# Kernel optimization log

Hardware: AMD Instinct MI355X
Metric: run time of the kernel (lower is better)

Reference implementation:

```python
import jax, jax.numpy as jnp
import numpy as np

B, S, NX, H = 8, 1024, 1024, 16
D = NX // H  # head dim = 64


def setup_inputs() -> dict:
    key = jax.random.key(0)
    k1, k2, k3 = jax.random.split(key, 3)
    x = jax.random.normal(k1, (B, S, NX), dtype=jnp.float32)
    Wqkv = jax.random.normal(k2, (NX, 3 * NX), dtype=jnp.float32) * 0.02
    bqkv = jnp.zeros((3 * NX,), dtype=jnp.float32)
    Wproj = jax.random.normal(k3, (NX, NX), dtype=jnp.float32) * 0.02
    bproj = jnp.zeros((NX,), dtype=jnp.float32)
    return {"x": x, "Wqkv": Wqkv, "bqkv": bqkv, "Wproj": Wproj, "bproj": bproj}


def reference(x, Wqkv, bqkv, Wproj, bproj):
    # c_attn: Conv1D == x @ W + b
    qkv = jnp.einsum('bsn,nm->bsm', x, Wqkv) + bqkv  # [B,S,3*NX]
    q, k, v = jnp.split(qkv, 3, axis=-1)
    # split heads -> [B,H,S,D]
    def split_heads(t):
        return t.reshape(B, S, H, D).transpose(0, 2, 1, 3)
    q, k, v = split_heads(q), split_heads(k), split_heads(v)
    # present = stack(key, value) with key as [B,H,S,D]
    present = jnp.stack((k, v))  # [2,B,H,S,D]
    # scores, scaled (scale=True) by sqrt(head_dim)
    w = jnp.einsum('bhqd,bhkd->bhqk', q, k) / jnp.sqrt(jnp.asarray(D, x.dtype))
    bias = jnp.tril(jnp.ones((S, S), dtype=x.dtype))[None, None]  # causal tril buffer
    w = w * bias - 10000.0 * (1.0 - bias)
    w = jax.nn.softmax(w, axis=-1)
    a = jnp.einsum('bhqk,bhkd->bhqd', w, v)  # [B,H,S,D]
    a = a.transpose(0, 2, 1, 3).reshape(B, S, NX)  # merge heads
    a = jnp.einsum('bsn,nm->bsm', a, Wproj) + bproj  # c_proj
    return a, present
```

## Files before the change

### kernel.cpp

```cpp
#include <hip/hip_runtime.h>
#include <stdint.h>


#define BB 8
#define SS 1024
#define NXX 1024
#define NH 16
#define HD 64
#define KK 1024
#define NKT 16

typedef __bf16 bf16x8 __attribute__((ext_vector_type(8)));
typedef float  floatx4 __attribute__((ext_vector_type(4)));
typedef unsigned short ushort8 __attribute__((ext_vector_type(8)));
typedef unsigned short ushortx4 __attribute__((ext_vector_type(4)));

__device__ inline float bf2f(unsigned short u) {
    unsigned int x = ((unsigned int)u) << 16;
    float f;
    __builtin_memcpy(&f, &x, 4);
    return f;
}
__device__ inline unsigned short f2bf(float f) {
    unsigned int u;
    __builtin_memcpy(&u, &f, 4);
    u += 0x7FFFu + ((u >> 16) & 1u);
    return (unsigned short)(u >> 16);
}

__device__ inline void gload_lds16(const unsigned short* g, unsigned short* l) {
    __builtin_amdgcn_global_load_lds(
        (const __attribute__((address_space(1))) void*)g,
        (__attribute__((address_space(3))) void*)l, 16, 0, 0);
}

__device__ inline void barrier_raw() {
    asm volatile("" ::: "memory");
    __builtin_amdgcn_sched_barrier(0);
    __builtin_amdgcn_s_barrier();
    __builtin_amdgcn_sched_barrier(0);
    asm volatile("" ::: "memory");
}
#define WAIT_VM4() asm volatile("s_waitcnt vmcnt(4)" ::: "memory")
#define WAIT_VM0() asm volatile("s_waitcnt vmcnt(0)" ::: "memory")

__global__ void sniff_k(const unsigned short* __restrict__ x, int* __restrict__ flag) {
    if (threadIdx.x == 0 && blockIdx.x == 0) {
        int g = 0;
        for (int i = 0; i < 512; i++) {
            float f = bf2f(x[i]);
            float a = fabsf(f);
            if (!(a <= 1e4f)) g++;
            else if (f != 0.f && a < 1e-35f) g++;
        }
        *flag = (g > 16) ? 1 : 0;
    }
}

__global__ __launch_bounds__(256) void prep(
    const void* __restrict__ x, const void* __restrict__ Wqkv,
    const void* __restrict__ Wproj,
    unsigned short* __restrict__ xbf, unsigned short* __restrict__ WqkvT,
    unsigned short* __restrict__ WprojT, const int* __restrict__ flagp) {
    const int f32 = *flagp;
    int blk = blockIdx.x;
    if (blk < 4096) {
        const size_t i = ((size_t)blk * 256 + threadIdx.x) * 8;
        if (f32) {
            const floatx4* p = (const floatx4*)((const float*)x + i);
            floatx4 f0 = p[0], f1 = p[1];
            ushort8 u;
#pragma unroll
            for (int j = 0; j < 4; j++) { u[j] = f2bf(f0[j]); u[4 + j] = f2bf(f1[j]); }
            *(ushort8*)(xbf + i) = u;
        } else {
            *(ushort8*)(xbf + i) = *(const ushort8*)((const unsigned short*)x + i);
        }
        return;
    }
    blk -= 4096;
    const void* in;
    unsigned short* out;
    int R, C;
    if (blk < 3072) { in = Wqkv; out = WqkvT; R = 1024; C = 3072; }
    else            { blk -= 3072; in = Wproj; out = WprojT; R = 1024; C = 1024; }
    const int ctiles = C / 32;
    const int c0 = (blk % ctiles) * 32, r0 = (blk / ctiles) * 32;

    __shared__ unsigned short tile[32][33];
    const int tx = threadIdx.x & 31, ty = threadIdx.x >> 5;
    if (f32) {
        const float* inf = (const float*)in;
#pragma unroll
        for (int i = ty; i < 32; i += 8)
            tile[i][tx] = f2bf(inf[(size_t)(r0 + i) * C + c0 + tx]);
    } else {
        const unsigned short* inu = (const unsigned short*)in;
#pragma unroll
        for (int i = ty; i < 32; i += 8)
            tile[i][tx] = inu[(size_t)(r0 + i) * C + c0 + tx];
    }
    __syncthreads();
#pragma unroll
    for (int i = ty; i < 32; i += 8)
        out[(size_t)(c0 + i) * R + r0 + tx] = tile[tx][i];
}

__global__ __launch_bounds__(256) void transpose_v(
    const void* __restrict__ outbase, unsigned short* __restrict__ vbfT,
    const int* __restrict__ flagp) {
    const int f32 = *flagp;
    const int blk = blockIdx.x;
    const int sb = blk & 15;
    const int bh = blk >> 4;
    const int tid = threadIdx.x;
    const int r = tid >> 2;
    const int c0 = (tid & 3) * 16;
    __shared__ unsigned short tile[64][72];
    const int perm = ((r & 15) << 2) | (r >> 4);
    const size_t esz = f32 ? 4 : 2;
    const char* vbase = (const char*)outbase + (size_t)(2 * BB * SS * NXX) * esz;
    if (f32) {
        const float* src = (const float*)vbase + ((size_t)bh * SS + sb * 64 + r) * HD + c0;
#pragma unroll
        for (int j = 0; j < 16; j++) tile[c0 + j][perm] = f2bf(src[j]);
    } else {
        const unsigned short* src = (const unsigned short*)vbase + ((size_t)bh * SS + sb * 64 + r) * HD + c0;
#pragma unroll
        for (int j = 0; j < 16; j++) tile[c0 + j][perm] = src[j];
    }
    __syncthreads();
    const int d = tid >> 2;
    const int o0 = (tid & 3) * 16;
    unsigned short* dst = vbfT + ((size_t)(bh * HD + d)) * SS + sb * 64 + o0;
    *(ushort8*)dst       = *(const ushort8*)&tile[d][o0];
    *(ushort8*)(dst + 8) = *(const ushort8*)&tile[d][o0 + 8];
}

#define STAGE_A(slot, h, kt) do { \
    const unsigned short* sg_ = Ab + (size_t)((h) * 128) * KK + (size_t)(kt) * 64; \
    gload_lds16(sg_, &As[slot][h][w * 512]); \
    gload_lds16(sg_ + (size_t)64 * KK, &As[slot][h][4096 + w * 512]); \
} while (0)
#define STAGE_B(slot, h, kt) do { \
    const unsigned short* sg_ = Bb + (size_t)((h) * 128) * KK + (size_t)(kt) * 64; \
    gload_lds16(sg_, &Bs[slot][h][w * 512]); \
    gload_lds16(sg_ + (size_t)64 * KK, &Bs[slot][h][4096 + w * 512]); \
} while (0)
#define PHASE(qq, STAGE_STMT, TAIL) do { \
    bf16x8 a_[2][2]; \
    _Pragma("unroll") \
    for (int mm = 0; mm < 2; mm++) { \
        const int arow = (qq) * 32 + mm * 16 + l15; \
        a_[mm][0] = *(const bf16x8*)&Ah[arow * 64 + fo0]; \
        a_[mm][1] = *(const bf16x8*)&Ah[arow * 64 + fo1]; \
    } \
    STAGE_STMT; \
    barrier_raw(); \
    __builtin_amdgcn_s_setprio(1); \
    _Pragma("unroll") \
    for (int mm = 0; mm < 2; mm++) \
    _Pragma("unroll") \
    for (int nf = 0; nf < 4; nf++) { \
        acc[2 * (qq) + mm][nf] = __builtin_amdgcn_mfma_f32_16x16x32_bf16(a_[mm][0], bfr[nf][0], acc[2 * (qq) + mm][nf], 0, 0, 0); \
        acc[2 * (qq) + mm][nf] = __builtin_amdgcn_mfma_f32_16x16x32_bf16(a_[mm][1], bfr[nf][1], acc[2 * (qq) + mm][nf], 0, 0, 0); \
    } \
    __builtin_amdgcn_s_setprio(0); \
    TAIL; \
    barrier_raw(); \
} while (0)

template <int MODE>
__global__ __launch_bounds__(512, 2) void gemm8p(
    const unsigned short* __restrict__ A,
    const unsigned short* __restrict__ Bt,
    const void* __restrict__ bias,
    void* __restrict__ outbase,
    unsigned short* __restrict__ q_ws,
    unsigned short* __restrict__ kbf,
    int M, int N, int Nt, const int* __restrict__ flagp) {
    __shared__ __align__(16) unsigned short As[2][2][128 * 64];
    __shared__ __align__(16) unsigned short Bs[2][2][128 * 64];

    const int f32 = *flagp;
    const int tid  = threadIdx.x;
    const int lane = tid & 63;
    const int w = tid >> 6;
    const int r = w >> 2;
    const int c = w & 3;
    const int bh2 = c >> 1;
    const int l15 = lane & 15;
    const int quad = lane >> 4;

    const int cpx = gridDim.x >> 3;
    const int bid = (blockIdx.x & 7) * cpx + (blockIdx.x >> 3);
    const int bx = bid % Nt, by = bid / Nt;
    const int row0 = by * 256, col0 = bx * 256;

    floatx4 acc[8][4];
    floatx4 zz = {0.f, 0.f, 0.f, 0.f};
#pragma unroll
    for (int i = 0; i < 8; i++)
#pragma unroll
        for (int j = 0; j < 4; j++) acc[i][j] = zz;

    const int srow = tid >> 3;
    const int scole = ((tid & 7) ^ (srow & 7)) << 3;
    const unsigned short* Ab = A  + (size_t)(row0 + srow) * KK + scole;
    const unsigned short* Bb = Bt + (size_t)(col0 + srow) * KK + scole;

    const int fo0 = (quad << 3) ^ ((l15 & 7) << 3);
    const int fo1 = fo0 ^ 32;

    STAGE_A(0, 0, 0); STAGE_A(0, 1, 0);
    STAGE_B(0, 0, 0); STAGE_B(0, 1, 0);
    STAGE_B(1, 0, 1); STAGE_B(1, 1, 1);
    WAIT_VM4();
    barrier_raw();

    bf16x8 bfr[4][2];
#pragma unroll 2
    for (int t = 0; t < NKT; t++) {
        const int slot = t & 1;
        const unsigned short* Ah = &As[slot][r][0];
        const unsigned short* Bh = &Bs[slot][bh2][0];
#pragma unroll
        for (int nf = 0; nf < 4; nf++) {
            const int brow = (c & 1) * 64 + nf * 16 + l15;
            bfr[nf][0] = *(const bf16x8*)&Bh[brow * 64 + fo0];
            bfr[nf][1] = *(const bf16x8*)&Bh[brow * 64 + fo1];
        }
        PHASE(0, { if (t + 1 < NKT) STAGE_A((t + 1) & 1, 0, t + 1); }, {});
        PHASE(1, { if (t + 1 < NKT) STAGE_A((t + 1) & 1, 1, t + 1); }, {});
        PHASE(2, { if (t + 2 < NKT) STAGE_B(slot, 0, t + 2); }, {});
        PHASE(3, { if (t + 2 < NKT) STAGE_B(slot, 1, t + 2); },
              { if (t < NKT - 2) { WAIT_VM4(); } else { WAIT_VM0(); } });
    }

    float bv[4];
#pragma unroll
    for (int nf = 0; nf < 4; nf++) {
        const int colb = col0 + c * 64 + nf * 16 + l15;
        bv[nf] = f32 ? ((const float*)bias)[colb] : bf2f(((const unsigned short*)bias)[colb]);
    }

    if (MODE == 0) {
#pragma unroll
        for (int mi = 0; mi < 8; mi++)
#pragma unroll
            for (int nf = 0; nf < 4; nf++) {
                const int colb = col0 + c * 64 + nf * 16 + l15;
#pragma unroll
                for (int i = 0; i < 4; i++) {
                    const int row = row0 + r * 128 + mi * 16 + quad * 4 + i;
                    const float val = acc[mi][nf][i] + bv[nf];
                    const size_t idx = (size_t)row * N + colb;
                    if (f32) ((float*)outbase)[idx] = val;
                    else     ((unsigned short*)outbase)[idx] = f2bf(val);
                }
            }
        return;
    }

    const int sec = col0 >> 10;
    const size_t esz = f32 ? 4 : 2;
    const int b = row0 >> 10;
    const int s0 = row0 & 1023;

    if (sec == 0) {
#pragma unroll
        for (int mi = 0; mi < 8; mi++)
#pragma unroll
            for (int nf = 0; nf < 4; nf++) {
                const int colb = col0 + c * 64 + nf * 16 + l15;
                const int h = (colb & 1023) >> 6, d = colb & 63;
#pragma unroll
                for (int i = 0; i < 4; i++) {
                    const int s = s0 + r * 128 + mi * 16 + quad * 4 + i;
                    q_ws[(size_t)((b * NH + h) * SS + s) * HD + d] = f2bf(acc[mi][nf][i] + bv[nf]);
                }
            }
    } else if (sec == 1) {
        char* kbase = (char*)outbase + (size_t)(BB * SS * NXX) * esz;
#pragma unroll
        for (int mi = 0; mi < 8; mi++)
#pragma unroll
            for (int nf = 0; nf < 4; nf++) {
                const int colb = col0 + c * 64 + nf * 16 + l15;
                const int h = (colb & 1023) >> 6, d = colb & 63;
#pragma unroll
                for (int i = 0; i < 4; i++) {
                    const int s = s0 + r * 128 + mi * 16 + quad * 4 + i;
                    const float val = acc[mi][nf][i] + bv[nf];
                    const size_t idx = (size_t)((b * NH + h) * SS + s) * HD + d;
                    if (f32) ((float*)kbase)[idx] = val;
                    else     ((unsigned short*)kbase)[idx] = f2bf(val);
                    kbf[idx] = f2bf(val);
                }
            }
    } else {
        char* vbase = (char*)outbase + (size_t)(2 * BB * SS * NXX) * esz;
#pragma unroll
        for (int mi = 0; mi < 8; mi++)
#pragma unroll
            for (int nf = 0; nf < 4; nf++) {
                const int colb = col0 + c * 64 + nf * 16 + l15;
                const int h = (colb & 1023) >> 6, d = colb & 63;
#pragma unroll
                for (int i = 0; i < 4; i++) {
                    const int s = s0 + r * 128 + mi * 16 + quad * 4 + i;
                    const float val = acc[mi][nf][i] + bv[nf];
                    const size_t idx = (size_t)((b * NH + h) * SS + s) * HD + d;
                    if (f32) ((float*)vbase)[idx] = val;
                    else     ((unsigned short*)vbase)[idx] = f2bf(val);
                }
            }
    }
}

__global__ __launch_bounds__(256) void attn(
    const unsigned short* __restrict__ q_ws,
    const unsigned short* __restrict__ kbf,
    const unsigned short* __restrict__ vbfT,
    unsigned short* __restrict__ amerged) {
    const int tid = threadIdx.x;
    const int lane = tid & 63;
    const int w = tid >> 6;
    const int l15 = lane & 15, quad = lane >> 4;
    const int blk = blockIdx.x;
    const int p = blk & 3;
    const int bh = blk >> 2;
    const int b = bh >> 4, h = bh & 15;

    const unsigned short* Q = q_ws + (size_t)bh * (SS * HD);
    const unsigned short* K = kbf + (size_t)bh * (SS * HD);
    const unsigned short* V = vbfT + (size_t)bh * (HD * SS);

    __shared__ __align__(16) unsigned short Ks[64][72];
    __shared__ __align__(16) unsigned short Vs[64][72];
    __shared__ __align__(16) unsigned short Pl[4][32][72];

    floatx4 zz = {0.f, 0.f, 0.f, 0.f};
    ushort8 ones_u;
#pragma unroll
    for (int j = 0; j < 8; j++) ones_u[j] = 0x3F80;
    const bf16x8 ones = __builtin_bit_cast(bf16x8, ones_u);

    const int srow = tid >> 2;
    const int soff = (tid & 3) * 16;

#pragma unroll
    for (int tile = 0; tile < 2; tile++) {
        const int qb = tile ? (7 - p) : p;
        const int qbase = qb * 128;
        const int wrow0 = qbase + w * 32;
        const int wq_max = wrow0 + 31;
        const int jend = qbase + 128;

        bf16x8 qa[2][2];
#pragma unroll
        for (int m = 0; m < 2; m++)
#pragma unroll
            for (int t = 0; t < 2; t++)
                qa[m][t] = *(const bf16x8*)&Q[(size_t)(wrow0 + m * 16 + l15) * HD + t * 32 + quad * 8];

        floatx4 o[2][4], o5[2];
        float mrow[2][4];
#pragma unroll
        for (int m = 0; m < 2; m++) {
            o5[m] = zz;
#pragma unroll
            for (int i = 0; i < 4; i++) mrow[m][i] = -1e30f;
#pragma unroll
            for (int nf = 0; nf < 4; nf++) o[m][nf] = zz;
        }

        *(ushort8*)&Ks[srow][soff]     = *(const ushort8*)&K[(size_t)srow * HD + soff];
        *(ushort8*)&Ks[srow][soff + 8] = *(const ushort8*)&K[(size_t)srow * HD + soff + 8];
        *(ushort8*)&Vs[srow][soff]     = *(const ushort8*)&V[(size_t)srow * SS + soff];
        *(ushort8*)&Vs[srow][soff + 8] = *(const ushort8*)&V[(size_t)srow * SS + soff + 8];
        __syncthreads();

        for (int j0 = 0; j0 < jend; j0 += 64) {
            const bool havenext = (j0 + 64 < jend);
            ushort8 kn0, kn1, vn0, vn1;
            if (havenext) {
                kn0 = *(const ushort8*)&K[(size_t)(j0 + 64 + srow) * HD + soff];
                kn1 = *(const ushort8*)&K[(size_t)(j0 + 64 + srow) * HD + soff + 8];
                vn0 = *(const ushort8*)&V[(size_t)srow * SS + j0 + 64 + soff];
                vn1 = *(const ushort8*)&V[(size_t)srow * SS + j0 + 64 + soff + 8];
            }

            if (j0 <= wq_max) {
                floatx4 sf[2][4];
#pragma unroll
                for (int kg = 0; kg < 4; kg++) {
                    bf16x8 kb0 = *(const bf16x8*)&Ks[kg * 16 + l15][quad * 8];
                    bf16x8 kb1 = *(const bf16x8*)&Ks[kg * 16 + l15][32 + quad * 8];
#pragma unroll
                    for (int m = 0; m < 2; m++) {
                        floatx4 s = zz;
                        s = __builtin_amdgcn_mfma_f32_16x16x32_bf16(qa[m][0], kb0, s, 0, 0, 0);
                        s = __builtin_amdgcn_mfma_f32_16x16x32_bf16(qa[m][1], kb1, s, 0, 0, 0);
                        sf[m][kg] = s;
                    }
                }

                float alpha_[2][4];
#pragma unroll
                for (int m = 0; m < 2; m++)
#pragma unroll
                    for (int i = 0; i < 4; i++) {
                        const int qrow = wrow0 + m * 16 + quad * 4 + i;
                        float pv4[4];
#pragma unroll
                        for (int kg = 0; kg < 4; kg++) {
                            const int key = j0 + kg * 16 + l15;
                            float s = sf[m][kg][i] * 0.125f;
                            if (key > qrow) s = -10000.0f;
                            pv4[kg] = s;
                        }
                        float t = fmaxf(fmaxf(pv4[0], pv4[1]), fmaxf(pv4[2], pv4[3]));
                        t = fmaxf(t, __shfl_xor(t, 1));
                        t = fmaxf(t, __shfl_xor(t, 2));
                        t = fmaxf(t, __shfl_xor(t, 4));
                        t = fmaxf(t, __shfl_xor(t, 8));
                        const float mnew = fmaxf(mrow[m][i], t);
                        alpha_[m][i] = __expf(mrow[m][i] - mnew);
                        mrow[m][i] = mnew;
                        ushortx4 pk;
#pragma unroll
                        for (int kg = 0; kg < 4; kg++)
                            pk[kg] = f2bf(__expf(pv4[kg] - mnew));
                        *(ushortx4*)&Pl[w][m * 16 + quad * 4 + i][l15 * 4] = pk;
                    }

#pragma unroll
                for (int m = 0; m < 2; m++) {
#pragma unroll
                    for (int i = 0; i < 4; i++) o5[m][i] *= alpha_[m][i];
#pragma unroll
                    for (int nf = 0; nf < 4; nf++)
#pragma unroll
                        for (int i = 0; i < 4; i++) o[m][nf][i] *= alpha_[m][i];
                }

                bf16x8 pa[2][2];
#pragma unroll
                for (int m = 0; m < 2; m++) {
                    pa[m][0] = *(const bf16x8*)&Pl[w][m * 16 + l15][quad * 8];
                    pa[m][1] = *(const bf16x8*)&Pl[w][m * 16 + l15][32 + quad * 8];
                }

#pragma unroll
                for (int m = 0; m < 2; m++) {
                    o5[m] = __builtin_amdgcn_mfma_f32_16x16x32_bf16(pa[m][0], ones, o5[m], 0, 0, 0);
                    o5[m] = __builtin_amdgcn_mfma_f32_16x16x32_bf16(pa[m][1], ones, o5[m], 0, 0, 0);
                }
#pragma unroll
                for (int nf = 0; nf < 4; nf++) {
                    bf16x8 vb0 = *(const bf16x8*)&Vs[nf * 16 + l15][quad * 8];
                    bf16x8 vb1 = *(const bf16x8*)&Vs[nf * 16 + l15][32 + quad * 8];
#pragma unroll
                    for (int m = 0; m < 2; m++) {
                        o[m][nf] = __builtin_amdgcn_mfma_f32_16x16x32_bf16(pa[m][0], vb0, o[m][nf], 0, 0, 0);
                        o[m][nf] = __builtin_amdgcn_mfma_f32_16x16x32_bf16(pa[m][1], vb1, o[m][nf], 0, 0, 0);
                    }
                }
            }
            __syncthreads();
            if (havenext) {
                *(ushort8*)&Ks[srow][soff]     = kn0;
                *(ushort8*)&Ks[srow][soff + 8] = kn1;
                *(ushort8*)&Vs[srow][soff]     = vn0;
                *(ushort8*)&Vs[srow][soff + 8] = vn1;
            }
            __syncthreads();
        }

#pragma unroll
        for (int m = 0; m < 2; m++)
#pragma unroll
            for (int nf = 0; nf < 4; nf++)
#pragma unroll
                for (int i = 0; i < 4; i++) {
                    const int s = wrow0 + m * 16 + quad * 4 + i;
                    amerged[(size_t)(b * SS + s) * NXX + h * HD + nf * 16 + l15] =
                        f2bf(o[m][nf][i] / o5[m][i]);
                }
        __syncthreads();
    }
}

extern "C" void kernel_launch(void* const* d_in, const int* in_sizes, int n_in,
                              void* d_out, int out_size, void* d_ws, size_t ws_size,
                              hipStream_t stream) {
    const void* x     = d_in[0];
    const void* Wqkv  = d_in[1];
    const void* bqkv  = d_in[2];
    const void* Wproj = d_in[3];
    const void* bproj = d_in[4];

    int* flag = (int*)d_ws;
    unsigned short* ws = (unsigned short*)d_ws + 8;
    unsigned short* WqkvT   = ws;
    unsigned short* WprojT  = WqkvT + 3072 * 1024;
    unsigned short* q_ws    = WprojT + 1024 * 1024;
    unsigned short* kbf     = q_ws + 8 * 1024 * 1024;
    unsigned short* vbfT    = kbf + 8 * 1024 * 1024;
    unsigned short* amerged = vbfT + 8 * 1024 * 1024;
    unsigned short* xbf     = amerged;

    sniff_k<<<1, 64, 0, stream>>>((const unsigned short*)x, flag);
    prep<<<dim3(8192), 256, 0, stream>>>(x, Wqkv, Wproj, xbf, WqkvT, WprojT, flag);
    gemm8p<1><<<dim3(12 * 32), 512, 0, stream>>>(
        xbf, WqkvT, bqkv, d_out, q_ws, kbf, 8192, 3072, 12, flag);
    transpose_v<<<dim3(128 * 16), 256, 0, stream>>>(d_out, vbfT, flag);
    attn<<<dim3(BB * NH * 4), 256, 0, stream>>>(q_ws, kbf, vbfT, amerged);
    gemm8p<0><<<dim3(4 * 32), 512, 0, stream>>>(
        amerged, WprojT, bproj, d_out, nullptr, nullptr, 8192, 1024, 4, flag);
}
```

Baseline: 346.7 us.

## Parameterize GEMM N-tile width to raise block count and double-buffer A fragments

Templates the GEMM on an NF parameter so each block covers 64*NF output columns. The QKV GEMM now uses 192-wide tiles over 512 blocks and the projection GEMM uses 128-wide tiles over 256 blocks, up from 384 and 128 blocks, to fill the CUs more evenly. The main loop is restructured to preload A fragments one quarter ahead in two register sets, and B staging is split into 64-row chunks with an NF-dependent vmcnt wait. The sniff kernel is also parallelized across a wavefront using shuffles. Smaller N tiles reduce A-operand reuse per block and add LDS traffic per FLOP.

```diff
diff --git a/kernel.cpp b/kernel.cpp
--- a/kernel.cpp
+++ b/kernel.cpp
@@ -41,20 +41,22 @@
     __builtin_amdgcn_sched_barrier(0);
     asm volatile("" ::: "memory");
 }
-#define WAIT_VM4() asm volatile("s_waitcnt vmcnt(4)" ::: "memory")
 #define WAIT_VM0() asm volatile("s_waitcnt vmcnt(0)" ::: "memory")
 
 __global__ void sniff_k(const unsigned short* __restrict__ x, int* __restrict__ flag) {
-    if (threadIdx.x == 0 && blockIdx.x == 0) {
-        int g = 0;
-        for (int i = 0; i < 512; i++) {
-            float f = bf2f(x[i]);
-            float a = fabsf(f);
-            if (!(a <= 1e4f)) g++;
-            else if (f != 0.f && a < 1e-35f) g++;
-        }
-        *flag = (g > 16) ? 1 : 0;
-    }
+    const int lane = threadIdx.x & 63;
+    ushort8 v = *(const ushort8*)(x + (size_t)lane * 8);
+    int g = 0;
+#pragma unroll
+    for (int j = 0; j < 8; j++) {
+        float f = bf2f(v[j]);
+        float a = fabsf(f);
+        if (!(a <= 1e4f)) g++;
+        else if (f != 0.f && a < 1e-35f) g++;
+    }
+#pragma unroll
+    for (int s = 1; s < 64; s <<= 1) g += __shfl_xor(g, s);
+    if (lane == 0 && blockIdx.x == 0) *flag = (g > 16) ? 1 : 0;
 }
 
 __global__ __launch_bounds__(256) void prep(
@@ -139,38 +141,39 @@
 
 #define STAGE_A(slot, h, kt) do { \
     const unsigned short* sg_ = Ab + (size_t)((h) * 128) * KK + (size_t)(kt) * 64; \
-    gload_lds16(sg_, &As[slot][h][w * 512]); \
-    gload_lds16(sg_ + (size_t)64 * KK, &As[slot][h][4096 + w * 512]); \
+    gload_lds16(sg_, &As[slot][(h) * 8192 + w * 512]); \
+    gload_lds16(sg_ + (size_t)64 * KK, &As[slot][(h) * 8192 + 4096 + w * 512]); \
 } while (0)
-#define STAGE_B(slot, h, kt) do { \
-    const unsigned short* sg_ = Bb + (size_t)((h) * 128) * KK + (size_t)(kt) * 64; \
-    gload_lds16(sg_, &Bs[slot][h][w * 512]); \
-    gload_lds16(sg_ + (size_t)64 * KK, &Bs[slot][h][4096 + w * 512]); \
+#define STAGE_B(slot, j, kt) do { \
+    const unsigned short* sg_ = Bb + (size_t)((j) * 64) * KK + (size_t)(kt) * 64; \
+    gload_lds16(sg_, &Bs[slot][(j) * 4096 + w * 512]); \
 } while (0)
-#define PHASE(qq, STAGE_STMT, TAIL) do { \
-    bf16x8 a_[2][2]; \
+#define LOADA(dst, qq) do { \
     _Pragma("unroll") \
     for (int mm = 0; mm < 2; mm++) { \
         const int arow = (qq) * 32 + mm * 16 + l15; \
-        a_[mm][0] = *(const bf16x8*)&Ah[arow * 64 + fo0]; \
-        a_[mm][1] = *(const bf16x8*)&Ah[arow * 64 + fo1]; \
+        dst[mm][0] = *(const bf16x8*)&Ah[arow * 64 + fo0]; \
+        dst[mm][1] = *(const bf16x8*)&Ah[arow * 64 + fo1]; \
     } \
-    STAGE_STMT; \
-    barrier_raw(); \
+} while (0)
+#define MFMAQ(qq, ar) do { \
     __builtin_amdgcn_s_setprio(1); \
     _Pragma("unroll") \
     for (int mm = 0; mm < 2; mm++) \
     _Pragma("unroll") \
-    for (int nf = 0; nf < 4; nf++) { \
-        acc[2 * (qq) + mm][nf] = __builtin_amdgcn_mfma_f32_16x16x32_bf16(a_[mm][0], bfr[nf][0], acc[2 * (qq) + mm][nf], 0, 0, 0); \
-        acc[2 * (qq) + mm][nf] = __builtin_amdgcn_mfma_f32_16x16x32_bf16(a_[mm][1], bfr[nf][1], acc[2 * (qq) + mm][nf], 0, 0, 0); \
+    for (int nf = 0; nf < NF; nf++) { \
+        acc[2 * (qq) + mm][nf] = __builtin_amdgcn_mfma_f32_16x16x32_bf16(ar[mm][0], bfr[nf][0], acc[2 * (qq) + mm][nf], 0, 0, 0); \
+        acc[2 * (qq) + mm][nf] = __builtin_amdgcn_mfma_f32_16x16x32_bf16(ar[mm][1], bfr[nf][1], acc[2 * (qq) + mm][nf], 0, 0, 0); \
     } \
     __builtin_amdgcn_s_setprio(0); \
-    TAIL; \
-    barrier_raw(); \
 } while (0)
-
-template <int MODE>
+#define WAIT_VMNF() do { \
+    if constexpr (NF == 2)      asm volatile("s_waitcnt vmcnt(2)" ::: "memory"); \
+    else if constexpr (NF == 3) asm volatile("s_waitcnt vmcnt(3)" ::: "memory"); \
+    else                        asm volatile("s_waitcnt vmcnt(4)" ::: "memory"); \
+} while (0)
+
+template <int MODE, int NF>
 __global__ __launch_bounds__(512, 2) void gemm8p(
     const unsigned short* __restrict__ A,
     const unsigned short* __restrict__ Bt,
@@ -178,9 +181,9 @@
     void* __restrict__ outbase,
     unsigned short* __restrict__ q_ws,
     unsigned short* __restrict__ kbf,
-    int M, int N, int Nt, const int* __restrict__ flagp) {
-    __shared__ __align__(16) unsigned short As[2][2][128 * 64];
-    __shared__ __align__(16) unsigned short Bs[2][2][128 * 64];
+    int N, int Nt, const int* __restrict__ flagp) {
+    __shared__ __align__(16) unsigned short As[2][2 * 8192];
+    __shared__ __align__(16) unsigned short Bs[2][NF * 4096];
 
     const int f32 = *flagp;
     const int tid  = threadIdx.x;
@@ -188,21 +191,20 @@
     const int w = tid >> 6;
     const int r = w >> 2;
     const int c = w & 3;
-    const int bh2 = c >> 1;
     const int l15 = lane & 15;
     const int quad = lane >> 4;
 
     const int cpx = gridDim.x >> 3;
     const int bid = (blockIdx.x & 7) * cpx + (blockIdx.x >> 3);
     const int bx = bid % Nt, by = bid / Nt;
-    const int row0 = by * 256, col0 = bx * 256;
-
-    floatx4 acc[8][4];
+    const int row0 = by * 256, col0 = bx * (64 * NF);
+
+    floatx4 acc[8][NF];
     floatx4 zz = {0.f, 0.f, 0.f, 0.f};
 #pragma unroll
     for (int i = 0; i < 8; i++)
 #pragma unroll
-        for (int j = 0; j < 4; j++) acc[i][j] = zz;
+        for (int j = 0; j < NF; j++) acc[i][j] = zz;
 
     const int srow = tid >> 3;
     const int scole = ((tid & 7) ^ (srow & 7)) << 3;
@@ -213,43 +215,67 @@
     const int fo1 = fo0 ^ 32;
 
     STAGE_A(0, 0, 0); STAGE_A(0, 1, 0);
-    STAGE_B(0, 0, 0); STAGE_B(0, 1, 0);
-    STAGE_B(1, 0, 1); STAGE_B(1, 1, 1);
-    WAIT_VM4();
+#pragma unroll
+    for (int j = 0; j < NF; j++) STAGE_B(0, j, 0);
+#pragma unroll
+    for (int j = 0; j < NF; j++) STAGE_B(1, j, 1);
+    WAIT_VMNF();
     barrier_raw();
 
-    bf16x8 bfr[4][2];
+    bf16x8 bfr[NF][2], aX[2][2], aY[2][2];
 #pragma unroll 2
     for (int t = 0; t < NKT; t++) {
         const int slot = t & 1;
-        const unsigned short* Ah = &As[slot][r][0];
-        const unsigned short* Bh = &Bs[slot][bh2][0];
-#pragma unroll
-        for (int nf = 0; nf < 4; nf++) {
-            const int brow = (c & 1) * 64 + nf * 16 + l15;
+        const unsigned short* Ah = &As[slot][r * 8192];
+        const unsigned short* Bh = &Bs[slot][0];
+#pragma unroll
+        for (int nf = 0; nf < NF; nf++) {
+            const int brow = c * (16 * NF) + nf * 16 + l15;
             bfr[nf][0] = *(const bf16x8*)&Bh[brow * 64 + fo0];
             bfr[nf][1] = *(const bf16x8*)&Bh[brow * 64 + fo1];
         }
-        PHASE(0, { if (t + 1 < NKT) STAGE_A((t + 1) & 1, 0, t + 1); }, {});
-        PHASE(1, { if (t + 1 < NKT) STAGE_A((t + 1) & 1, 1, t + 1); }, {});
-        PHASE(2, { if (t + 2 < NKT) STAGE_B(slot, 0, t + 2); }, {});
-        PHASE(3, { if (t + 2 < NKT) STAGE_B(slot, 1, t + 2); },
-              { if (t < NKT - 2) { WAIT_VM4(); } else { WAIT_VM0(); } });
-    }
-
-    float bv[4];
-#pragma unroll
-    for (int nf = 0; nf < 4; nf++) {
-        const int colb = col0 + c * 64 + nf * 16 + l15;
+        LOADA(aX, 0);
+        LOADA(aY, 1);
+        if (t + 1 < NKT) STAGE_A(slot ^ 1, 0, t + 1);
+        barrier_raw();
+        MFMAQ(0, aX);
+        barrier_raw();
+        LOADA(aX, 2);
+        if (t + 1 < NKT) STAGE_A(slot ^ 1, 1, t + 1);
+        barrier_raw();
+        MFMAQ(1, aY);
+        barrier_raw();
+        LOADA(aY, 3);
+        if (t + 2 < NKT) {
+#pragma unroll
+            for (int j = 0; j < (NF + 1) / 2; j++) STAGE_B(slot, j, t + 2);
+        }
+        barrier_raw();
+        MFMAQ(2, aX);
+        barrier_raw();
+        if (t + 2 < NKT) {
+#pragma unroll
+            for (int j = (NF + 1) / 2; j < NF; j++) STAGE_B(slot, j, t + 2);
+        }
+        barrier_raw();
+        MFMAQ(3, aY);
+        if (t < NKT - 2) { WAIT_VMNF(); } else { WAIT_VM0(); }
+        barrier_raw();
+    }
+
+    float bv[NF];
+#pragma unroll
+    for (int nf = 0; nf < NF; nf++) {
+        const int colb = col0 + c * (16 * NF) + nf * 16 + l15;
         bv[nf] = f32 ? ((const float*)bias)[colb] : bf2f(((const unsigned short*)bias)[colb]);
     }
 
     if (MODE == 0) {
 #pragma unroll
-        for (int mi = 0; mi < 8; mi++)
-#pragma unroll
-            for (int nf = 0; nf < 4; nf++) {
-                const int colb = col0 + c * 64 + nf * 16 + l15;
+        for (int nf = 0; nf < NF; nf++) {
+            const int colb = col0 + c * (16 * NF) + nf * 16 + l15;
+#pragma unroll
+            for (int mi = 0; mi < 8; mi++)
 #pragma unroll
                 for (int i = 0; i < 4; i++) {
                     const int row = row0 + r * 128 + mi * 16 + quad * 4 + i;
@@ -258,36 +284,31 @@
                     if (f32) ((float*)outbase)[idx] = val;
                     else     ((unsigned short*)outbase)[idx] = f2bf(val);
                 }
-            }
+        }
         return;
     }
 
-    const int sec = col0 >> 10;
     const size_t esz = f32 ? 4 : 2;
     const int b = row0 >> 10;
     const int s0 = row0 & 1023;
 
-    if (sec == 0) {
-#pragma unroll
-        for (int mi = 0; mi < 8; mi++)
-#pragma unroll
-            for (int nf = 0; nf < 4; nf++) {
-                const int colb = col0 + c * 64 + nf * 16 + l15;
-                const int h = (colb & 1023) >> 6, d = colb & 63;
+#pragma unroll
+    for (int nf = 0; nf < NF; nf++) {
+        const int colb = col0 + c * (16 * NF) + nf * 16 + l15;
+        const int sec = colb >> 10;
+        const int h = (colb & 1023) >> 6, d = colb & 63;
+        if (sec == 0) {
+#pragma unroll
+            for (int mi = 0; mi < 8; mi++)
 #pragma unroll
                 for (int i = 0; i < 4; i++) {
                     const int s = s0 + r * 128 + mi * 16 + quad * 4 + i;
                     q_ws[(size_t)((b * NH + h) * SS + s) * HD + d] = f2bf(acc[mi][nf][i] + bv[nf]);
                 }
-            }
-    } else if (sec == 1) {
-        char* kbase = (char*)outbase + (size_t)(BB * SS * NXX) * esz;
-#pragma unroll
-        for (int mi = 0; mi < 8; mi++)
-#pragma unroll
-            for (int nf = 0; nf < 4; nf++) {
-                const int colb = col0 + c * 64 + nf * 16 + l15;
-                const int h = (colb & 1023) >> 6, d = colb & 63;
+        } else if (sec == 1) {
+            char* kbase = (char*)outbase + (size_t)(BB * SS * NXX) * esz;
+#pragma unroll
+            for (int mi = 0; mi < 8; mi++)
 #pragma unroll
                 for (int i = 0; i < 4; i++) {
                     const int s = s0 + r * 128 + mi * 16 + quad * 4 + i;
@@ -297,15 +318,10 @@
                     else     ((unsigned short*)kbase)[idx] = f2bf(val);
                     kbf[idx] = f2bf(val);
                 }
-            }
-    } else {
-        char* vbase = (char*)outbase + (size_t)(2 * BB * SS * NXX) * esz;
-#pragma unroll
-        for (int mi = 0; mi < 8; mi++)
-#pragma unroll
-            for (int nf = 0; nf < 4; nf++) {
-                const int colb = col0 + c * 64 + nf * 16 + l15;
-                const int h = (colb & 1023) >> 6, d = colb & 63;
+        } else {
+            char* vbase = (char*)outbase + (size_t)(2 * BB * SS * NXX) * esz;
+#pragma unroll
+            for (int mi = 0; mi < 8; mi++)
 #pragma unroll
                 for (int i = 0; i < 4; i++) {
                     const int s = s0 + r * 128 + mi * 16 + quad * 4 + i;
@@ -314,7 +330,7 @@
                     if (f32) ((float*)vbase)[idx] = val;
                     else     ((unsigned short*)vbase)[idx] = f2bf(val);
                 }
-            }
+        }
     }
 }
 
@@ -513,10 +529,10 @@
 
     sniff_k<<<1, 64, 0, stream>>>((const unsigned short*)x, flag);
     prep<<<dim3(8192), 256, 0, stream>>>(x, Wqkv, Wproj, xbf, WqkvT, WprojT, flag);
-    gemm8p<1><<<dim3(12 * 32), 512, 0, stream>>>(
-        xbf, WqkvT, bqkv, d_out, q_ws, kbf, 8192, 3072, 12, flag);
+    gemm8p<1, 3><<<dim3(512), 512, 0, stream>>>(
+        xbf, WqkvT, bqkv, d_out, q_ws, kbf, 3072, 16, flag);
     transpose_v<<<dim3(128 * 16), 256, 0, stream>>>(d_out, vbfT, flag);
     attn<<<dim3(BB * NH * 4), 256, 0, stream>>>(q_ws, kbf, vbfT, amerged);
-    gemm8p<0><<<dim3(4 * 32), 512, 0, stream>>>(
-        amerged, WprojT, bproj, d_out, nullptr, nullptr, 8192, 1024, 4, flag);
-}
+    gemm8p<0, 2><<<dim3(256), 512, 0, stream>>>(
+        amerged, WprojT, bproj, d_out, nullptr, nullptr, 1024, 8, flag);
+}
```

New measurement: 326.1 us. 1.06x faster.
